# Kernel optimization log

Hardware: AMD Instinct MI355X
Metric: run time of the kernel (lower is better)

The kernel has to match this reference:

```python
import jax, jax.numpy as jnp
import numpy as np

DM, H, DK = 768, 12, 64

def setup_inputs() -> dict:
    key = jax.random.key(0)
    ks = jax.random.split(key, 12)
    B, S = 6, 1024
    sc = 1.0 / np.sqrt(DM)
    return {
        "Q": jax.random.normal(ks[0], (B, S, DM), jnp.float32),
        "K": jax.random.normal(ks[1], (B, S, DM), jnp.float32),
        "V": jax.random.normal(ks[2], (B, S, DM), jnp.float32),
        "attn_mask": jax.random.randint(ks[3], (B, S, S), 0, 2) > 0,
        "W_q": jax.random.uniform(ks[4], (DM, H * DK), jnp.float32, -sc, sc),
        "b_q": jax.random.uniform(ks[5], (H * DK,), jnp.float32, -sc, sc),
        "W_k": jax.random.uniform(ks[6], (DM, H * DK), jnp.float32, -sc, sc),
        "b_k": jax.random.uniform(ks[7], (H * DK,), jnp.float32, -sc, sc),
        "W_v": jax.random.uniform(ks[8], (DM, H * DK), jnp.float32, -sc, sc),
        "b_v": jax.random.uniform(ks[9], (H * DK,), jnp.float32, -sc, sc),
        "W_o": jax.random.uniform(ks[10], (H * DK, DM), jnp.float32, -1/np.sqrt(H*DK), 1/np.sqrt(H*DK)),
        "b_o": jax.random.uniform(ks[11], (DM,), jnp.float32, -1/np.sqrt(H*DK), 1/np.sqrt(H*DK)),
        "gamma": jnp.ones((DM,), jnp.float32),
        "beta": jnp.zeros((DM,), jnp.float32),
    }

def reference(Q, K, V, attn_mask, W_q, b_q, W_k, b_k, W_v, b_v, W_o, b_o, gamma, beta):
    B, S, _ = Q.shape
    residual = Q
    # projections -> [B, H, S, DK]
    q = (Q @ W_q + b_q).reshape(B, S, H, DK).transpose(0, 2, 1, 3)
    k = (K @ W_k + b_k).reshape(B, S, H, DK).transpose(0, 2, 1, 3)
    v = (V @ W_v + b_v).reshape(B, S, H, DK).transpose(0, 2, 1, 3)
    scores = jnp.einsum('bhqd,bhkd->bhqk', q, k) / np.sqrt(DK)
    scores = jnp.where(attn_mask[:, None, :, :], -1e9, scores)
    attn = jax.nn.softmax(scores, axis=-1)
    context = jnp.einsum('bhqk,bhkd->bhqd', attn, v)
    context = context.transpose(0, 2, 1, 3).reshape(B, S, H * DK)
    output = context @ W_o + b_o
    x = output + residual
    mu = jnp.mean(x, axis=-1, keepdims=True)
    var = jnp.var(x, axis=-1, keepdims=True)
    out = (x - mu) / jnp.sqrt(var + 1e-5) * gamma + beta
    return out, attn
```

## Files before the change

kernel.cpp:

```cpp
#include <hip/hip_runtime.h>
#include <hip/hip_bf16.h>

#define B 6
#define S 1024
#define H 12
#define DK 64
#define DM 768
#define M (B*S)
#define BH (B*H)

typedef __bf16 bf16;
typedef __attribute__((ext_vector_type(8))) __bf16 bf16x8;
typedef __attribute__((ext_vector_type(4))) float f32x4;

#define MFMA __builtin_amdgcn_mfma_f32_16x16x32_bf16

__device__ __forceinline__ void lds_barrier() {
  asm volatile("s_waitcnt lgkmcnt(0)" ::: "memory");
  __builtin_amdgcn_s_barrier();
}

__global__ void k_prep(const float* __restrict__ Q, const float* __restrict__ K,
                       const float* __restrict__ V,
                       const float* __restrict__ Wq, const float* __restrict__ Wk,
                       const float* __restrict__ Wv, const float* __restrict__ Wo,
                       bf16* __restrict__ xb, bf16* __restrict__ wt) {
  int z = blockIdx.y;
  if (z < 3) {
    const float* X = z==0?Q : z==1?K : V;
    size_t i = ((size_t)blockIdx.x*256 + threadIdx.x)*8;
    float4 a = *(const float4*)(X + i);
    float4 b = *(const float4*)(X + i + 4);
    bf16x8 r;
    r[0]=(bf16)a.x; r[1]=(bf16)a.y; r[2]=(bf16)a.z; r[3]=(bf16)a.w;
    r[4]=(bf16)b.x; r[5]=(bf16)b.y; r[6]=(bf16)b.z; r[7]=(bf16)b.w;
    *(bf16x8*)(xb + (size_t)z*M*DM + i) = r;
  } else {
    int zz = z - 3;
    const float* W = zz==0?Wq : zz==1?Wk : zz==2?Wv : Wo;
    int idx = blockIdx.x*256 + threadIdx.x;
    int k = idx / DM, n = idx % DM;
    wt[(size_t)zz*DM*DM + (size_t)n*DM + k] = (bf16)W[idx];
  }
}


__global__ __launch_bounds__(256, 3) void k_proj(
    const bf16* __restrict__ xb, const bf16* __restrict__ wt,
    const float* __restrict__ bq, const float* __restrict__ bk,
    const float* __restrict__ bv,
    bf16* __restrict__ qb, bf16* __restrict__ kb, bf16* __restrict__ vt) {
  int z = blockIdx.z;
  const bf16* X    = xb + (size_t)z*M*DM;
  const float* bias = z==0?bq : z==1?bk : bv;
  const bf16* Wt = wt + (size_t)z*DM*DM;
  int tid = threadIdx.x, lane = tid & 63, w = tid >> 6;
  int wr = w >> 1, wc = w & 1;
  int lr = lane & 15, lg = lane >> 4;
  int m0 = blockIdx.x*128;
  int n0 = blockIdx.y*128;

  __shared__ bf16 As[2][128*32];
  __shared__ bf16 Bs[2][128*32];

  const int srow = tid >> 1;
  const int c0   = (tid & 1) * 2;
  const int f    = (srow >> 1) & 3;
  const int sc   = (c0 ^ f) & ~1;
  const bool sw  = (f & 1);
  const bf16* asrc = X  + (size_t)(m0 + srow)*DM + sc*8;
  const bf16* bsrc = Wt + (size_t)(n0 + srow)*DM + sc*8;
  const int dst0 = srow*32 + c0*8;

  const int fs = (lr >> 1) & 3;
  const int fchunk = (lg ^ fs) * 8;

  f32x4 acc[4][4];
  #pragma unroll
  for (int i=0;i<4;++i)
    #pragma unroll
    for (int j=0;j<4;++j) acc[i][j] = (f32x4){0.f,0.f,0.f,0.f};

  {
    bf16x8 a0 = *(const bf16x8*)(asrc);
    bf16x8 a1 = *(const bf16x8*)(asrc + 8);
    bf16x8 b0 = *(const bf16x8*)(bsrc);
    bf16x8 b1 = *(const bf16x8*)(bsrc + 8);
    *(bf16x8*)&As[0][dst0]     = sw ? a1 : a0;
    *(bf16x8*)&As[0][dst0 + 8] = sw ? a0 : a1;
    *(bf16x8*)&Bs[0][dst0]     = sw ? b1 : b0;
    *(bf16x8*)&Bs[0][dst0 + 8] = sw ? b0 : b1;
  }
  lds_barrier();

  for (int t = 0; t < 24; ++t) {
    int cur = t & 1;
    bf16x8 pa0, pa1, pb0, pb1;
    if (t < 23) {
      int k0 = (t+1)*32;
      pa0 = *(const bf16x8*)(asrc + k0);
      pa1 = *(const bf16x8*)(asrc + k0 + 8);
      pb0 = *(const bf16x8*)(bsrc + k0);
      pb1 = *(const bf16x8*)(bsrc + k0 + 8);
    }
    bf16x8 af[4], bfr[4];
    #pragma unroll
    for (int mi=0;mi<4;++mi) af[mi]  = *(const bf16x8*)&As[cur][(wr*64 + mi*16 + lr)*32 + fchunk];
    #pragma unroll
    for (int ni=0;ni<4;++ni) bfr[ni] = *(const bf16x8*)&Bs[cur][(wc*64 + ni*16 + lr)*32 + fchunk];
    #pragma unroll
    for (int mi=0;mi<4;++mi)
      #pragma unroll
      for (int ni=0;ni<4;++ni)
        acc[mi][ni] = MFMA(af[mi], bfr[ni], acc[mi][ni], 0,0,0);
    if (t < 23) {
      *(bf16x8*)&As[cur^1][dst0]     = sw ? pa1 : pa0;
      *(bf16x8*)&As[cur^1][dst0 + 8] = sw ? pa0 : pa1;
      *(bf16x8*)&Bs[cur^1][dst0]     = sw ? pb1 : pb0;
      *(bf16x8*)&Bs[cur^1][dst0 + 8] = sw ? pb0 : pb1;
      lds_barrier();
    }
  }

  int mw = m0 + wr*64, nw = n0 + wc*64;
  #pragma unroll
  for (int ni=0;ni<4;++ni) {
    int n = nw + ni*16 + lr;
    float bs = bias[n];
    int h = n >> 6, d = n & 63;
    #pragma unroll
    for (int mi=0;mi<4;++mi)
      #pragma unroll
      for (int r=0;r<4;++r) {
        int m = mw + mi*16 + lg*4 + r;
        int bb = m >> 10, s = m & 1023;
        float val = acc[mi][ni][r] + bs;
        if (z == 0) {
          qb[((size_t)(bb*H + h)*S + s)*DK + d] = (bf16)val;
        } else if (z == 1) {
          int dsw = ((((d>>3) ^ (s&7))) << 3) | (d&7);
          kb[((size_t)(bb*H + h)*S + s)*DK + dsw] = (bf16)val;
        } else {
          int ssw = (s & ~63) | ((((s&63)>>3) ^ (d&7)) << 3) | (s&7);
          vt[((size_t)(bb*H + h)*DK + d)*S + ssw] = (bf16)val;
        }
      }
  }
}

__global__ __launch_bounds__(256, 3) void k_oproj(
    const bf16* __restrict__ ctx, const bf16* __restrict__ wto,
    const float* __restrict__ bo, const float* __restrict__ res,
    float* __restrict__ x) {
  int tid = threadIdx.x, lane = tid & 63, w = tid >> 6;
  int wr = w >> 1, wc = w & 1;
  int lr = lane & 15, lg = lane >> 4;
  int m0 = blockIdx.x*128;
  int n0 = blockIdx.y*128;

  __shared__ bf16 As[2][128*32];
  __shared__ bf16 Bs[2][128*32];

  const int srow = tid >> 1;
  const int c0   = (tid & 1) * 2;
  const int f    = (srow >> 1) & 3;
  const int sc   = (c0 ^ f) & ~1;
  const bool sw  = (f & 1);
  const bf16* asrc = ctx + (size_t)(m0 + srow)*DM + sc*8;
  const bf16* bsrc = wto + (size_t)(n0 + srow)*DM + sc*8;
  const int dst0 = srow*32 + c0*8;
  const int fs = (lr >> 1) & 3;
  const int fchunk = (lg ^ fs) * 8;

  f32x4 acc[4][4];
  #pragma unroll
  for (int i=0;i<4;++i)
    #pragma unroll
    for (int j=0;j<4;++j) acc[i][j] = (f32x4){0.f,0.f,0.f,0.f};

  {
    bf16x8 a0 = *(const bf16x8*)(asrc);
    bf16x8 a1 = *(const bf16x8*)(asrc + 8);
    bf16x8 b0 = *(const bf16x8*)(bsrc);
    bf16x8 b1 = *(const bf16x8*)(bsrc + 8);
    *(bf16x8*)&As[0][dst0]     = sw ? a1 : a0;
    *(bf16x8*)&As[0][dst0 + 8] = sw ? a0 : a1;
    *(bf16x8*)&Bs[0][dst0]     = sw ? b1 : b0;
    *(bf16x8*)&Bs[0][dst0 + 8] = sw ? b0 : b1;
  }
  lds_barrier();

  for (int t = 0; t < 24; ++t) {
    int cur = t & 1;
    bf16x8 pa0, pa1, pb0, pb1;
    if (t < 23) {
      int k0 = (t+1)*32;
      pa0 = *(const bf16x8*)(asrc + k0);
      pa1 = *(const bf16x8*)(asrc + k0 + 8);
      pb0 = *(const bf16x8*)(bsrc + k0);
      pb1 = *(const bf16x8*)(bsrc + k0 + 8);
    }
    bf16x8 af[4], bfr[4];
    #pragma unroll
    for (int mi=0;mi<4;++mi) af[mi]  = *(const bf16x8*)&As[cur][(wr*64 + mi*16 + lr)*32 + fchunk];
    #pragma unroll
    for (int ni=0;ni<4;++ni) bfr[ni] = *(const bf16x8*)&Bs[cur][(wc*64 + ni*16 + lr)*32 + fchunk];
    #pragma unroll
    for (int mi=0;mi<4;++mi)
      #pragma unroll
      for (int ni=0;ni<4;++ni)
        acc[mi][ni] = MFMA(af[mi], bfr[ni], acc[mi][ni], 0,0,0);
    if (t < 23) {
      *(bf16x8*)&As[cur^1][dst0]     = sw ? pa1 : pa0;
      *(bf16x8*)&As[cur^1][dst0 + 8] = sw ? pa0 : pa1;
      *(bf16x8*)&Bs[cur^1][dst0]     = sw ? pb1 : pb0;
      *(bf16x8*)&Bs[cur^1][dst0 + 8] = sw ? pb0 : pb1;
      lds_barrier();
    }
  }

  int mw = m0 + wr*64, nw = n0 + wc*64;
  #pragma unroll
  for (int ni=0;ni<4;++ni) {
    int n = nw + ni*16 + lr;
    float bb = bo[n];
    #pragma unroll
    for (int mi=0;mi<4;++mi)
      #pragma unroll
      for (int r=0;r<4;++r) {
        int m = mw + mi*16 + lg*4 + r;
        x[(size_t)m*DM + n] = acc[mi][ni][r] + bb + res[(size_t)m*DM + n];
      }
  }
}

__device__ __forceinline__ unsigned pk2(float a, float b) {
  union { bf16 h[2]; unsigned u; } x;
  x.h[0] = (bf16)a; x.h[1] = (bf16)b;
  return x.u;
}

__global__ __launch_bounds__(256, 4) void k_fattn(
    const bf16* __restrict__ qb, const bf16* __restrict__ kb,
    const bf16* __restrict__ vt, const unsigned char* __restrict__ mask,
    float* __restrict__ attn, bf16* __restrict__ ctx) {
  int lin = blockIdx.x + 16*blockIdx.y;
  int xcd  = lin & 7;
  int slot = lin >> 3;
  int qt   = slot & 15;
  int bh   = xcd*9 + (slot >> 4);
  int b = bh / H, h = bh - b*H;
  int tid = threadIdx.x, lane = tid & 63, w = tid >> 6;
  int lr = lane & 15, lg = lane >> 4;
  int q0 = qt*64 + w*16;

  __shared__ bf16 Kb[2][4096];
  __shared__ bf16 Vb[2][4096];
  __shared__ bf16 pt[4][2][512];

  const bf16* qbase = qb + ((size_t)bh*S + q0 + lr)*DK + lg*8;
  bf16x8 qa0 = *(const bf16x8*)(qbase);
  bf16x8 qa1 = *(const bf16x8*)(qbase + 32);

  const char* kg = (const char*)(kb + (size_t)bh*S*DK);
  const char* vg = (const char*)(vt + (size_t)bh*DK*S);
  const unsigned char* mrow = mask + ((size_t)b*S + q0 + lr)*S;
  float* abase = attn + ((size_t)bh*S + q0 + lr)*S;

  const int koff0 = w*2048 + lane*16, koff1 = koff0 + 1024;
  const int kd0 = w*1024 + lane*8,    kd1 = kd0 + 512;
  const int vrow0 = w*16 + (lane>>3), vrow1 = vrow0 + 8;
  const int vcb = (lane&7)*16;
  const int vd0 = vrow0*64 + (lane&7)*8, vd1 = vd0 + 512;

  const int krow = lr*64;
  const int kf0o = krow + ((lg ^ (lr&7))<<3);
  const int kf1o = krow + (((4+lg) ^ (lr&7))<<3);
  const int swz  = (lr & 3) << 4;

  {
    bf16x8 a0 = *(const bf16x8*)(kg + koff0);
    bf16x8 a1 = *(const bf16x8*)(kg + koff1);
    *(bf16x8*)&Kb[0][kd0] = a0;
    *(bf16x8*)&Kb[0][kd1] = a1;
  }
  uchar4 mkn[4];
  #pragma unroll
  for (int i=0;i<4;++i) mkn[i] = *(const uchar4*)(mrow + i*16 + lg*4);
  lds_barrier();

  float sum = 0.f;
  for (int t = 0; t < 16; ++t) {
    int cur = t & 1;
    uchar4 mkc[4];
    #pragma unroll
    for (int i=0;i<4;++i) mkc[i] = mkn[i];
    bf16x8 kn0, kn1;
    if (t < 15) {
      kn0 = *(const bf16x8*)(kg + (t+1)*8192 + koff0);
      kn1 = *(const bf16x8*)(kg + (t+1)*8192 + koff1);
      #pragma unroll
      for (int i=0;i<4;++i) mkn[i] = *(const uchar4*)(mrow + (t+1)*64 + i*16 + lg*4);
    }
    #pragma unroll
    for (int i=0;i<4;++i) {
      bf16x8 kf0 = *(const bf16x8*)&Kb[cur][i*1024 + kf0o];
      bf16x8 kf1 = *(const bf16x8*)&Kb[cur][i*1024 + kf1o];
      f32x4 sc = {0.f,0.f,0.f,0.f};
      sc = MFMA(kf0, qa0, sc, 0,0,0);
      sc = MFMA(kf1, qa1, sc, 0,0,0);
      sum += mkc[i].x ? 0.f : __expf(sc[0]*0.125f);
      sum += mkc[i].y ? 0.f : __expf(sc[1]*0.125f);
      sum += mkc[i].z ? 0.f : __expf(sc[2]*0.125f);
      sum += mkc[i].w ? 0.f : __expf(sc[3]*0.125f);
    }
    if (t < 15) {
      *(bf16x8*)&Kb[cur^1][kd0] = kn0;
      *(bf16x8*)&Kb[cur^1][kd1] = kn1;
    }
    lds_barrier();
  }
  sum += __shfl_xor(sum, 16);
  sum += __shfl_xor(sum, 32);
  float inv = 1.f / sum;

  f32x4 cacc[4];
  #pragma unroll
  for (int d=0;d<4;++d) cacc[d] = (f32x4){0.f,0.f,0.f,0.f};

  {
    bf16x8 a0 = *(const bf16x8*)(kg + koff0);
    bf16x8 a1 = *(const bf16x8*)(kg + koff1);
    bf16x8 b0 = *(const bf16x8*)(vg + (size_t)vrow0*2048 + vcb);
    bf16x8 b1 = *(const bf16x8*)(vg + (size_t)vrow1*2048 + vcb);
    *(bf16x8*)&Kb[0][kd0] = a0;
    *(bf16x8*)&Kb[0][kd1] = a1;
    *(bf16x8*)&Vb[0][vd0] = b0;
    *(bf16x8*)&Vb[0][vd1] = b1;
    #pragma unroll
    for (int i=0;i<4;++i) mkn[i] = *(const uchar4*)(mrow + i*16 + lg*4);
  }
  lds_barrier();

  for (int t = 0; t < 16; ++t) {
    int cur = t & 1;
    uchar4 mkc[4];
    #pragma unroll
    for (int i=0;i<4;++i) mkc[i] = mkn[i];
    bf16x8 kn0, kn1, vn0, vn1;
    if (t < 15) {
      kn0 = *(const bf16x8*)(kg + (t+1)*8192 + koff0);
      kn1 = *(const bf16x8*)(kg + (t+1)*8192 + koff1);
      vn0 = *(const bf16x8*)(vg + (size_t)vrow0*2048 + (t+1)*128 + vcb);
      vn1 = *(const bf16x8*)(vg + (size_t)vrow1*2048 + (t+1)*128 + vcb);
      #pragma unroll
      for (int i=0;i<4;++i) mkn[i] = *(const uchar4*)(mrow + (t+1)*64 + i*16 + lg*4);
    }
    #pragma unroll
    for (int u = 0; u < 2; ++u) {
      char* buf = (char*)&pt[w][u][0];
      #pragma unroll
      for (int half = 0; half < 2; ++half) {
        int i = u*2 + half;
        bf16x8 kf0 = *(const bf16x8*)&Kb[cur][i*1024 + kf0o];
        bf16x8 kf1 = *(const bf16x8*)&Kb[cur][i*1024 + kf1o];
        f32x4 sc = {0.f,0.f,0.f,0.f};
        sc = MFMA(kf0, qa0, sc, 0,0,0);
        sc = MFMA(kf1, qa1, sc, 0,0,0);
        float p0 = mkc[i].x ? 0.f : __expf(sc[0]*0.125f)*inv;
        float p1 = mkc[i].y ? 0.f : __expf(sc[1]*0.125f)*inv;
        float p2 = mkc[i].z ? 0.f : __expf(sc[2]*0.125f)*inv;
        float p3 = mkc[i].w ? 0.f : __expf(sc[3]*0.125f)*inv;
        *(float4*)(abase + t*64 + i*16 + lg*4) = (float4){p0,p1,p2,p3};
        uint2 pw2; pw2.x = pk2(p0,p1); pw2.y = pk2(p2,p3);
        *(uint2*)(buf + lr*64 + ((half*32 + lg*8) ^ swz)) = pw2;
      }
      bf16x8 pa = *(const bf16x8*)(buf + lr*64 + ((lg*16) ^ swz));
      #pragma unroll
      for (int dd=0; dd<4; ++dd) {
        bf16x8 vf = *(const bf16x8*)&Vb[cur][dd*1024 + lr*64 + ((((u*4+lg) ^ (lr&7)))<<3)];
        cacc[dd] = MFMA(pa, vf, cacc[dd], 0,0,0);
      }
    }
    if (t < 15) {
      *(bf16x8*)&Kb[cur^1][kd0] = kn0;
      *(bf16x8*)&Kb[cur^1][kd1] = kn1;
      *(bf16x8*)&Vb[cur^1][vd0] = vn0;
      *(bf16x8*)&Vb[cur^1][vd1] = vn1;
    }
    lds_barrier();
  }

  #pragma unroll
  for (int d=0;d<4;++d)
    #pragma unroll
    for (int r=0;r<4;++r)
      ctx[((size_t)b*S + q0 + lg*4 + r)*DM + h*DK + d*16 + lr] = (bf16)cacc[d][r];
}

__global__ void k_ln(const float* __restrict__ x, const float* __restrict__ gamma,
                     const float* __restrict__ beta, float* __restrict__ out) {
  int row = blockIdx.x; int tid = threadIdx.x;
  const float* xr = x + (size_t)row*DM;
  float v0 = xr[tid], v1 = xr[tid+256], v2 = xr[tid+512];
  float s = v0+v1+v2, ss = v0*v0+v1*v1+v2*v2;
  #pragma unroll
  for (int off=32; off; off>>=1){ s += __shfl_xor(s,off); ss += __shfl_xor(ss,off); }
  __shared__ float sm[8];
  int w = tid>>6;
  if ((tid&63)==0){ sm[w]=s; sm[4+w]=ss; }
  __syncthreads();
  s = sm[0]+sm[1]+sm[2]+sm[3]; ss = sm[4]+sm[5]+sm[6]+sm[7];
  float mean = s * (1.f/DM);
  float var = ss * (1.f/DM) - mean*mean;
  float rstd = rsqrtf(var + 1e-5f);
  out[(size_t)row*DM + tid]     = (v0-mean)*rstd*gamma[tid]     + beta[tid];
  out[(size_t)row*DM + tid+256] = (v1-mean)*rstd*gamma[tid+256] + beta[tid+256];
  out[(size_t)row*DM + tid+512] = (v2-mean)*rstd*gamma[tid+512] + beta[tid+512];
}

extern "C" void kernel_launch(void* const* d_in, const int* in_sizes, int n_in,
                              void* d_out, int out_size, void* d_ws, size_t ws_size,
                              hipStream_t stream) {
  const float* Q  = (const float*)d_in[0];
  const float* K  = (const float*)d_in[1];
  const float* V  = (const float*)d_in[2];
  const unsigned char* mask = (const unsigned char*)d_in[3];
  const float* Wq = (const float*)d_in[4];
  const float* bq = (const float*)d_in[5];
  const float* Wk = (const float*)d_in[6];
  const float* bk = (const float*)d_in[7];
  const float* Wv = (const float*)d_in[8];
  const float* bv = (const float*)d_in[9];
  const float* Wo = (const float*)d_in[10];
  const float* bo = (const float*)d_in[11];
  const float* gamma = (const float*)d_in[12];
  const float* beta  = (const float*)d_in[13];

  char* ws = (char*)d_ws;
  bf16* wt  = (bf16*)(ws + 0);
  bf16* xb  = (bf16*)(ws + 4718592);
  bf16* qb  = (bf16*)(ws + 33030144);
  bf16* kb  = (bf16*)(ws + 42467328);
  bf16* vt  = (bf16*)(ws + 51904512);
  bf16* ctx = (bf16*)(ws + 61341696);
  float* x  = (float*)(ws + 4718592);

  float* out  = (float*)d_out;
  float* attn = out + (size_t)B*S*DM;

  k_prep  <<<dim3(2304,7),  256, 0, stream>>>(Q,K,V,Wq,Wk,Wv,Wo,xb,wt);
  k_proj  <<<dim3(48,6,3),  256, 0, stream>>>(xb,wt,bq,bk,bv,qb,kb,vt);
  k_fattn <<<dim3(16,BH),   256, 0, stream>>>(qb,kb,vt,mask,attn,ctx);
  k_oproj <<<dim3(48,6),    256, 0, stream>>>(ctx, wt + (size_t)3*DM*DM, bo, Q, x);
  k_ln    <<<dim3(M),       256, 0, stream>>>(x,gamma,beta,out);
}
```

Measured before the change: 251.6 us.

## Restructure attention kernel with direct global-to-LDS K staging and register-held V

Moves K-tile staging from register round-trips to global_load_lds async copies with 128-key tiles and vmcnt-based waits instead of lgkmcnt barriers. V fragments are now loaded straight from global memory into registers in the MFMA fragment layout and double-buffered across half-tiles, which removes the V LDS buffer. Folds the 1/sqrt(dk)·log2(e) scale into Q at projection time so softmax uses exp2f without a multiply, and adds sched_barrier and setprio hints to keep the MFMA/exp sections grouped. The hand-counted vmcnt waits are fragile, and the extra V registers raise register pressure at four waves per SIMD.

After: 382.3 us. 52.0% more time.

```diff
diff --git a/kernel.cpp b/kernel.cpp
--- a/kernel.cpp
+++ b/kernel.cpp
@@ -14,11 +14,22 @@
 typedef __attribute__((ext_vector_type(4))) float f32x4;
 
 #define MFMA __builtin_amdgcn_mfma_f32_16x16x32_bf16
+#define SFENCE() __builtin_amdgcn_sched_barrier(0)
+#define WAITV(N) asm volatile("s_waitcnt vmcnt(" #N ")" ::: "memory")
+#define BARRIER() __builtin_amdgcn_s_barrier()
 
 __device__ __forceinline__ void lds_barrier() {
   asm volatile("s_waitcnt lgkmcnt(0)" ::: "memory");
   __builtin_amdgcn_s_barrier();
 }
+
+__device__ __forceinline__ void gl16(const void* g, void* l) {
+  __builtin_amdgcn_global_load_lds(
+      (const __attribute__((address_space(1))) unsigned int*)g,
+      (__attribute__((address_space(3))) unsigned int*)l, 16, 0, 0);
+}
+
+#define QSCALE 0.18033688011112042f
 
 __global__ void k_prep(const float* __restrict__ Q, const float* __restrict__ K,
                        const float* __restrict__ V,
@@ -44,7 +55,6 @@
   }
 }
 
-
 __global__ __launch_bounds__(256, 3) void k_proj(
     const bf16* __restrict__ xb, const bf16* __restrict__ wt,
     const float* __restrict__ bq, const float* __restrict__ bk,
@@ -71,7 +81,6 @@
   const bf16* asrc = X  + (size_t)(m0 + srow)*DM + sc*8;
   const bf16* bsrc = Wt + (size_t)(n0 + srow)*DM + sc*8;
   const int dst0 = srow*32 + c0*8;
-
   const int fs = (lr >> 1) & 3;
   const int fchunk = (lg ^ fs) * 8;
 
@@ -136,7 +145,7 @@
         int bb = m >> 10, s = m & 1023;
         float val = acc[mi][ni][r] + bs;
         if (z == 0) {
-          qb[((size_t)(bb*H + h)*S + s)*DK + d] = (bf16)val;
+          qb[((size_t)(bb*H + h)*S + s)*DK + d] = (bf16)(val * QSCALE);
         } else if (z == 1) {
           int dsw = ((((d>>3) ^ (s&7))) << 3) | (d&7);
           kb[((size_t)(bb*H + h)*S + s)*DK + dsw] = (bf16)val;
@@ -239,6 +248,51 @@
   x.h[0] = (bf16)a; x.h[1] = (bf16)b;
   return x.u;
 }
+
+
+#define STAGE_K(T, BUF)                                                        \
+  gl16(ksrc + (T)*16384,         KbL + (BUF)*16384 + ldsK);                    \
+  gl16(ksrc + (T)*16384 + 4096,  KbL + (BUF)*16384 + ldsK + 4096);             \
+  gl16(ksrc + (T)*16384 + 8192,  KbL + (BUF)*16384 + ldsK + 8192);             \
+  gl16(ksrc + (T)*16384 + 12288, KbL + (BUF)*16384 + ldsK + 12288);
+
+#define FSUB(T, KOFF, VC, VN, MC, MN)                                          \
+  {                                                                            \
+    const bf16* Kt = (const bf16*)(KbL + (KOFF));                              \
+    if ((T) < 15) {                                                            \
+      _Pragma("unroll")                                                        \
+      for (int j=0;j<8;++j) VN[j] = *(const bf16x8*)(vg + voff[j] + ((T)+1)*128); \
+      _Pragma("unroll")                                                        \
+      for (int i=0;i<4;++i) MN[i] = *(const uchar4*)(mrow + ((T)+1)*64 + i*16 + lg*4); \
+    }                                                                          \
+    SFENCE();                                                                  \
+    __builtin_amdgcn_s_setprio(1);                                             \
+    _Pragma("unroll")                                                          \
+    for (int u = 0; u < 2; ++u) {                                              \
+      _Pragma("unroll")                                                        \
+      for (int hf = 0; hf < 2; ++hf) {                                         \
+        int i = u*2 + hf;                                                      \
+        bf16x8 kf0 = *(const bf16x8*)&Kt[i*1024 + kf0o];                       \
+        bf16x8 kf1 = *(const bf16x8*)&Kt[i*1024 + kf1o];                       \
+        f32x4 sc = {0.f,0.f,0.f,0.f};                                          \
+        sc = MFMA(kf0, qa0, sc, 0,0,0);                                        \
+        sc = MFMA(kf1, qa1, sc, 0,0,0);                                        \
+        float p0 = MC[i].x ? 0.f : exp2f(sc[0])*inv;                           \
+        float p1 = MC[i].y ? 0.f : exp2f(sc[1])*inv;                           \
+        float p2 = MC[i].z ? 0.f : exp2f(sc[2])*inv;                           \
+        float p3 = MC[i].w ? 0.f : exp2f(sc[3])*inv;                           \
+        *(float4*)(abase + (T)*64 + i*16 + lg*4) = (float4){p0,p1,p2,p3};      \
+        uint2 pw2; pw2.x = pk2(p0,p1); pw2.y = pk2(p2,p3);                     \
+        *(uint2*)(buf + lr*64 + ((hf*32 + lg*8) ^ swzP)) = pw2;                \
+      }                                                                        \
+      bf16x8 pa = *(const bf16x8*)(buf + lr*64 + ((lg*16) ^ swzP));            \
+      _Pragma("unroll")                                                        \
+      for (int dd=0; dd<4; ++dd)                                               \
+        cacc[dd] = MFMA(pa, VC[u*4+dd], cacc[dd], 0,0,0);                      \
+    }                                                                          \
+    __builtin_amdgcn_s_setprio(0);                                             \
+    SFENCE();                                                                  \
+  }
 
 __global__ __launch_bounds__(256, 4) void k_fattn(
     const bf16* __restrict__ qb, const bf16* __restrict__ kb,
@@ -254,71 +308,74 @@
   int lr = lane & 15, lg = lane >> 4;
   int q0 = qt*64 + w*16;
 
-  __shared__ bf16 Kb[2][4096];
-  __shared__ bf16 Vb[2][4096];
-  __shared__ bf16 pt[4][2][512];
+  __shared__ bf16 Kb[2][8192];
+  __shared__ bf16 pt[4][512];
+  char* KbL = (char*)&Kb[0][0];
+  char* buf = (char*)&pt[w][0];
 
   const bf16* qbase = qb + ((size_t)bh*S + q0 + lr)*DK + lg*8;
   bf16x8 qa0 = *(const bf16x8*)(qbase);
   bf16x8 qa1 = *(const bf16x8*)(qbase + 32);
+  SFENCE();
 
   const char* kg = (const char*)(kb + (size_t)bh*S*DK);
   const char* vg = (const char*)(vt + (size_t)bh*DK*S);
   const unsigned char* mrow = mask + ((size_t)b*S + q0 + lr)*S;
   float* abase = attn + ((size_t)bh*S + q0 + lr)*S;
 
-  const int koff0 = w*2048 + lane*16, koff1 = koff0 + 1024;
-  const int kd0 = w*1024 + lane*8,    kd1 = kd0 + 512;
-  const int vrow0 = w*16 + (lane>>3), vrow1 = vrow0 + 8;
-  const int vcb = (lane&7)*16;
-  const int vd0 = vrow0*64 + (lane&7)*8, vd1 = vd0 + 512;
+  const char* ksrc = kg + w*1024 + lane*16;
+  const int ldsK = w*1024;
+
+  int voff[8];
+  #pragma unroll
+  for (int u=0;u<2;++u)
+    #pragma unroll
+    for (int dd=0;dd<4;++dd)
+      voff[u*4+dd] = (dd*16+lr)*2048 + ((((u*4+lg) ^ (lr&7))) << 4);
 
   const int krow = lr*64;
   const int kf0o = krow + ((lg ^ (lr&7))<<3);
   const int kf1o = krow + (((4+lg) ^ (lr&7))<<3);
-  const int swz  = (lr & 3) << 4;
-
-  {
-    bf16x8 a0 = *(const bf16x8*)(kg + koff0);
-    bf16x8 a1 = *(const bf16x8*)(kg + koff1);
-    *(bf16x8*)&Kb[0][kd0] = a0;
-    *(bf16x8*)&Kb[0][kd1] = a1;
-  }
-  uchar4 mkn[4];
-  #pragma unroll
-  for (int i=0;i<4;++i) mkn[i] = *(const uchar4*)(mrow + i*16 + lg*4);
-  lds_barrier();
+  const int swzP = (lr & 3) << 4;
+
+  STAGE_K(0, 0);
+  SFENCE();
+  uchar4 mkc[8], mkn[8];
+  #pragma unroll
+  for (int i=0;i<8;++i) mkn[i] = *(const uchar4*)(mrow + i*16 + lg*4);
+  SFENCE();
+  WAITV(8);
+  BARRIER();
+  SFENCE();
 
   float sum = 0.f;
-  for (int t = 0; t < 16; ++t) {
-    int cur = t & 1;
-    uchar4 mkc[4];
-    #pragma unroll
-    for (int i=0;i<4;++i) mkc[i] = mkn[i];
-    bf16x8 kn0, kn1;
-    if (t < 15) {
-      kn0 = *(const bf16x8*)(kg + (t+1)*8192 + koff0);
-      kn1 = *(const bf16x8*)(kg + (t+1)*8192 + koff1);
+  for (int t = 0; t < 8; ++t) {
+    const bf16* Kt = (const bf16*)(KbL + (t&1)*16384);
+    if (t < 7) { STAGE_K(t+1, (t+1)&1); }
+    SFENCE();
+    #pragma unroll
+    for (int i=0;i<8;++i) mkc[i] = mkn[i];
+    if (t < 7) {
       #pragma unroll
-      for (int i=0;i<4;++i) mkn[i] = *(const uchar4*)(mrow + (t+1)*64 + i*16 + lg*4);
-    }
-    #pragma unroll
-    for (int i=0;i<4;++i) {
-      bf16x8 kf0 = *(const bf16x8*)&Kb[cur][i*1024 + kf0o];
-      bf16x8 kf1 = *(const bf16x8*)&Kb[cur][i*1024 + kf1o];
+      for (int i=0;i<8;++i) mkn[i] = *(const uchar4*)(mrow + (t+1)*128 + i*16 + lg*4);
+    }
+    SFENCE();
+    __builtin_amdgcn_s_setprio(1);
+    #pragma unroll
+    for (int i=0;i<8;++i) {
+      bf16x8 kf0 = *(const bf16x8*)&Kt[i*1024 + kf0o];
+      bf16x8 kf1 = *(const bf16x8*)&Kt[i*1024 + kf1o];
       f32x4 sc = {0.f,0.f,0.f,0.f};
       sc = MFMA(kf0, qa0, sc, 0,0,0);
       sc = MFMA(kf1, qa1, sc, 0,0,0);
-      sum += mkc[i].x ? 0.f : __expf(sc[0]*0.125f);
-      sum += mkc[i].y ? 0.f : __expf(sc[1]*0.125f);
-      sum += mkc[i].z ? 0.f : __expf(sc[2]*0.125f);
-      sum += mkc[i].w ? 0.f : __expf(sc[3]*0.125f);
-    }
-    if (t < 15) {
-      *(bf16x8*)&Kb[cur^1][kd0] = kn0;
-      *(bf16x8*)&Kb[cur^1][kd1] = kn1;
-    }
-    lds_barrier();
+      sum += mkc[i].x ? 0.f : exp2f(sc[0]);
+      sum += mkc[i].y ? 0.f : exp2f(sc[1]);
+      sum += mkc[i].z ? 0.f : exp2f(sc[2]);
+      sum += mkc[i].w ? 0.f : exp2f(sc[3]);
+    }
+    __builtin_amdgcn_s_setprio(0);
+    SFENCE();
+    if (t < 7) { WAITV(8); BARRIER(); SFENCE(); }
   }
   sum += __shfl_xor(sum, 16);
   sum += __shfl_xor(sum, 32);
@@ -327,68 +384,26 @@
   f32x4 cacc[4];
   #pragma unroll
   for (int d=0;d<4;++d) cacc[d] = (f32x4){0.f,0.f,0.f,0.f};
-
-  {
-    bf16x8 a0 = *(const bf16x8*)(kg + koff0);
-    bf16x8 a1 = *(const bf16x8*)(kg + koff1);
-    bf16x8 b0 = *(const bf16x8*)(vg + (size_t)vrow0*2048 + vcb);
-    bf16x8 b1 = *(const bf16x8*)(vg + (size_t)vrow1*2048 + vcb);
-    *(bf16x8*)&Kb[0][kd0] = a0;
-    *(bf16x8*)&Kb[0][kd1] = a1;
-    *(bf16x8*)&Vb[0][vd0] = b0;
-    *(bf16x8*)&Vb[0][vd1] = b1;
-    #pragma unroll
-    for (int i=0;i<4;++i) mkn[i] = *(const uchar4*)(mrow + i*16 + lg*4);
-  }
-  lds_barrier();
-
-  for (int t = 0; t < 16; ++t) {
-    int cur = t & 1;
-    uchar4 mkc[4];
-    #pragma unroll
-    for (int i=0;i<4;++i) mkc[i] = mkn[i];
-    bf16x8 kn0, kn1, vn0, vn1;
-    if (t < 15) {
-      kn0 = *(const bf16x8*)(kg + (t+1)*8192 + koff0);
-      kn1 = *(const bf16x8*)(kg + (t+1)*8192 + koff1);
-      vn0 = *(const bf16x8*)(vg + (size_t)vrow0*2048 + (t+1)*128 + vcb);
-      vn1 = *(const bf16x8*)(vg + (size_t)vrow1*2048 + (t+1)*128 + vcb);
-      #pragma unroll
-      for (int i=0;i<4;++i) mkn[i] = *(const uchar4*)(mrow + (t+1)*64 + i*16 + lg*4);
-    }
-    #pragma unroll
-    for (int u = 0; u < 2; ++u) {
-      char* buf = (char*)&pt[w][u][0];
-      #pragma unroll
-      for (int half = 0; half < 2; ++half) {
-        int i = u*2 + half;
-        bf16x8 kf0 = *(const bf16x8*)&Kb[cur][i*1024 + kf0o];
-        bf16x8 kf1 = *(const bf16x8*)&Kb[cur][i*1024 + kf1o];
-        f32x4 sc = {0.f,0.f,0.f,0.f};
-        sc = MFMA(kf0, qa0, sc, 0,0,0);
-        sc = MFMA(kf1, qa1, sc, 0,0,0);
-        float p0 = mkc[i].x ? 0.f : __expf(sc[0]*0.125f)*inv;
-        float p1 = mkc[i].y ? 0.f : __expf(sc[1]*0.125f)*inv;
-        float p2 = mkc[i].z ? 0.f : __expf(sc[2]*0.125f)*inv;
-        float p3 = mkc[i].w ? 0.f : __expf(sc[3]*0.125f)*inv;
-        *(float4*)(abase + t*64 + i*16 + lg*4) = (float4){p0,p1,p2,p3};
-        uint2 pw2; pw2.x = pk2(p0,p1); pw2.y = pk2(p2,p3);
-        *(uint2*)(buf + lr*64 + ((half*32 + lg*8) ^ swz)) = pw2;
-      }
-      bf16x8 pa = *(const bf16x8*)(buf + lr*64 + ((lg*16) ^ swz));
-      #pragma unroll
-      for (int dd=0; dd<4; ++dd) {
-        bf16x8 vf = *(const bf16x8*)&Vb[cur][dd*1024 + lr*64 + ((((u*4+lg) ^ (lr&7)))<<3)];
-        cacc[dd] = MFMA(pa, vf, cacc[dd], 0,0,0);
-      }
-    }
-    if (t < 15) {
-      *(bf16x8*)&Kb[cur^1][kd0] = kn0;
-      *(bf16x8*)&Kb[cur^1][kd1] = kn1;
-      *(bf16x8*)&Vb[cur^1][vd0] = vn0;
-      *(bf16x8*)&Vb[cur^1][vd1] = vn1;
-    }
-    lds_barrier();
+  bf16x8 VA[8], VB[8];
+  uchar4 mkA[4], mkB[4];
+
+  STAGE_K(0, 0);
+  SFENCE();
+  #pragma unroll
+  for (int j=0;j<8;++j) VA[j] = *(const bf16x8*)(vg + voff[j]);
+  #pragma unroll
+  for (int i=0;i<4;++i) mkA[i] = *(const uchar4*)(mrow + i*16 + lg*4);
+  SFENCE();
+  WAITV(12);
+  BARRIER();
+  SFENCE();
+
+  for (int t = 0; t < 8; ++t) {
+    if (t < 7) { STAGE_K(t+1, (t+1)&1); }
+    SFENCE();
+    FSUB(2*t,   (t&1)*16384,        VA, VB, mkA, mkB);
+    FSUB(2*t+1, (t&1)*16384 + 8192, VB, VA, mkB, mkA);
+    if (t < 7) { WAITV(32); BARRIER(); SFENCE(); }
   }
 
   #pragma unroll
```
